# Performance work log

Hardware: AMD Instinct MI355X
Metric: run time of the kernel (lower is better)

## Reference

```python
import jax, jax.numpy as jnp
import numpy as np

N_HEADS = 16

def setup_inputs() -> dict:
    key = jax.random.key(0)
    k1, k2, k3 = jax.random.split(key, 3)
    B, T, C = 4, 2048, 1024
    x = jax.random.normal(k1, (B, T, C), dtype=jnp.float32)
    w_qkv = jax.random.normal(k2, (C, 3 * C), dtype=jnp.float32) * (1.0 / np.sqrt(C))
    w_out = jax.random.normal(k3, (C, C), dtype=jnp.float32) * (1.0 / np.sqrt(C))
    return {"x": x, "w_qkv": w_qkv, "w_out": w_out}

def reference(x, w_qkv, w_out):
    B, T, C = x.shape
    H = N_HEADS
    d_k = C // H
    qkv = x @ w_qkv                       # (B,T,3C)
    q, k, v = jnp.split(qkv, 3, axis=-1)
    # (B,H,T,d_k)
    q = q.reshape(B, T, H, d_k).transpose(0, 2, 1, 3)
    k = k.reshape(B, T, H, d_k).transpose(0, 2, 1, 3)
    v = v.reshape(B, T, H, d_k).transpose(0, 2, 1, 3)
    scale = 1.0 / np.sqrt(d_k)
    scores = jnp.einsum('bhqd,bhkd->bhqk', q, k) * scale  # (B,H,T,T)
    causal = jnp.triu(jnp.ones((T, T), dtype=bool), k=1)  # True = ignore
    scores = jnp.where(causal, -jnp.inf, scores)
    weights = jax.nn.softmax(scores, axis=-1)
    out = jnp.einsum('bhqk,bhkd->bhqd', weights, v)       # (B,H,T,d_k)
    out = out.transpose(0, 2, 1, 3).reshape(B, T, C)
    return out @ w_out
```

## Files before the change

kernel.cpp:

```cpp
#include <hip/hip_runtime.h>
#include <hip/hip_bf16.h>
#include <stdint.h>
#include <math.h>

typedef __bf16 bf16;
typedef __bf16 bf16x4 __attribute__((ext_vector_type(4)));
typedef __bf16 bf16x8 __attribute__((ext_vector_type(8)));
typedef float f32x4 __attribute__((ext_vector_type(4)));

#define BB 4
#define TT 2048
#define CC 1024
#define HH 16
#define DK 64

__device__ __forceinline__ void gl_lds16(const void* gsrc, void* ldst) {
    __builtin_amdgcn_global_load_lds(
        (__attribute__((address_space(1))) void*)(void*)(gsrc),
        (__attribute__((address_space(3))) void*)(ldst),
        16, 0, 0);
}

__global__ __launch_bounds__(256) void prep(
    const float* __restrict__ x, const float* __restrict__ wq,
    const float* __restrict__ wo, bf16* __restrict__ xbf,
    bf16* __restrict__ wqT, bf16* __restrict__ woT) {
    __shared__ bf16 tile[32][33];
    const int bid = blockIdx.x, tid = threadIdx.x;
    if (bid < 4096) {
        const int i = (bid * 256 + tid) * 8;
        const f32x4 a = *(const f32x4*)(x + i);
        const f32x4 b = *(const f32x4*)(x + i + 4);
        bf16x8 o;
#pragma unroll
        for (int j = 0; j < 4; ++j) { o[j] = (bf16)a[j]; o[j + 4] = (bf16)b[j]; }
        *(bf16x8*)(xbf + i) = o;
        return;
    }
    const float* in;
    bf16* out;
    int R, C, c0, r0;
    if (bid < 7168) {
        const int tb = bid - 4096;
        in = wq; out = wqT; R = 1024; C = 3072;
        c0 = (tb % 96) * 32; r0 = (tb / 96) * 32;
    } else {
        const int tb = bid - 7168;
        in = wo; out = woT; R = 1024; C = 1024;
        c0 = (tb % 32) * 32; r0 = (tb / 32) * 32;
    }
    const int tx = tid & 31, ty = tid >> 5;
#pragma unroll
    for (int i = 0; i < 32; i += 8)
        tile[ty + i][tx] = (bf16)in[(size_t)(r0 + ty + i) * C + c0 + tx];
    __syncthreads();
#pragma unroll
    for (int i = 0; i < 32; i += 8)
        out[(size_t)(c0 + ty + i) * R + r0 + tx] = tile[tx][ty + i];
}

template <int EPI>
__global__ __launch_bounds__(256) void gemm_bt(
    const bf16* __restrict__ A, const bf16* __restrict__ Bt,
    void* __restrict__ Cq, bf16* __restrict__ Kh, bf16* __restrict__ Vt,
    int M, int N, int K) {
    __shared__ bf16 As[128 * 32];
    __shared__ bf16 Bs[128 * 32];
    const int tid = threadIdx.x;
    const int w = tid >> 6, l = tid & 63;
    const int wm = w >> 1, wn = w & 1;
    const int m0 = blockIdx.y * 128, n0 = blockIdx.x * 128;
    const int lr4 = l >> 2, lc4 = (l & 3) * 8;
    const int lm = l & 15, lq = l >> 4;

    f32x4 acc[4][4] = {};

    for (int k0 = 0; k0 < K; k0 += 32) {
#pragma unroll
        for (int i = 0; i < 2; ++i) {
            const int j = w * 2 + i;
            gl_lds16(A + (size_t)(m0 + j * 16 + lr4) * K + k0 + lc4, As + j * 512);
            gl_lds16(Bt + (size_t)(n0 + j * 16 + lr4) * K + k0 + lc4, Bs + j * 512);
        }
        __syncthreads();
        bf16x8 af[4], bfr[4];
#pragma unroll
        for (int mi = 0; mi < 4; ++mi)
            af[mi] = *(const bf16x8*)(As + (wm * 64 + mi * 16 + lm) * 32 + lq * 8);
#pragma unroll
        for (int ni = 0; ni < 4; ++ni)
            bfr[ni] = *(const bf16x8*)(Bs + (wn * 64 + ni * 16 + lm) * 32 + lq * 8);
#pragma unroll
        for (int mi = 0; mi < 4; ++mi)
#pragma unroll
            for (int ni = 0; ni < 4; ++ni)
                acc[mi][ni] = __builtin_amdgcn_mfma_f32_16x16x32_bf16(
                    af[mi], bfr[ni], acc[mi][ni], 0, 0, 0);
        __syncthreads();
    }

    if (EPI == 0) {
#pragma unroll
        for (int mi = 0; mi < 4; ++mi) {
            const int row = m0 + wm * 64 + mi * 16 + lq * 4;
#pragma unroll
            for (int ni = 0; ni < 4; ++ni) {
                const int col = n0 + wn * 64 + ni * 16 + lm;
#pragma unroll
                for (int r = 0; r < 4; ++r)
                    ((float*)Cq)[(size_t)(row + r) * N + col] = acc[mi][ni][r];
            }
        }
    } else {
        bf16* Q = (bf16*)Cq;
#pragma unroll
        for (int ni = 0; ni < 4; ++ni) {
            const int c = n0 + wn * 64 + ni * 16 + lm;
            const int part = c >> 10;
            const int h = (c & 1023) >> 6;
            const int d = c & 63;
#pragma unroll
            for (int mi = 0; mi < 4; ++mi) {
                const int rowg = m0 + wm * 64 + mi * 16 + lq * 4;
#pragma unroll
                for (int r = 0; r < 4; ++r) {
                    const int rg = rowg + r;
                    const int b = rg >> 11, t = rg & 2047;
                    const bf16 v = (bf16)acc[mi][ni][r];
                    if (part == 0)
                        Q[((size_t)(b * HH + h) * TT + t) * DK + d] = v;
                    else if (part == 1)
                        Kh[((size_t)(b * HH + h) * TT + t) * DK + d] = v;
                    else
                        Vt[((size_t)(b * HH + h) * DK + d) * TT + t] = v;
                }
            }
        }
    }
}

#define PAD 72
__global__ __launch_bounds__(256, 3) void attn_kernel(
    const bf16* __restrict__ Qh, const bf16* __restrict__ Kh,
    const bf16* __restrict__ Vt, bf16* __restrict__ O) {
    __shared__ bf16 Ks[2][64 * PAD];
    __shared__ bf16 Vs[2][64 * PAD];
    __shared__ bf16 Ps[64 * PAD];
    const int tid = threadIdx.x, w = tid >> 6, l = tid & 63;
    const int lm = l & 15, lq = l >> 4;
    const int id = blockIdx.x;
    const int xcd = id & 7;
    const int rest = id >> 3;
    const int bh = xcd + 8 * (rest >> 4);
    const int p = rest & 15;
    const int b = bh >> 4, h = bh & 15;
    const bf16* Qb = Qh + (size_t)bh * TT * DK;
    const bf16* Kb = Kh + (size_t)bh * TT * DK;
    const bf16* Vb = Vt + (size_t)bh * DK * TT;
    const int srow = tid >> 3, scol = (tid & 7) * 8;

    const float smul = 0.125f * 1.44269504088896340736f;
    const int qts[2] = {p, 31 - p};

    bf16x8 kreg[2], vreg[2];
#pragma unroll
    for (int i = 0; i < 2; ++i) {
        kreg[i] = *(const bf16x8*)(Kb + (size_t)(srow + i * 32) * DK + scol);
        vreg[i] = *(const bf16x8*)(Vb + (size_t)(srow + i * 32) * TT + scol);
    }
    int buf = 0;

#pragma unroll
    for (int half = 0; half < 2; ++half) {
        const int qt = qts[half];
        const int q0 = qt * 64;
        const int qg = q0 + w * 16 + lm;

        bf16x8 qf[2];
#pragma unroll
        for (int ks = 0; ks < 2; ++ks)
            qf[ks] = *(const bf16x8*)(Qb + (size_t)(q0 + w * 16 + lm) * DK +
                                      ks * 32 + lq * 8);

        f32x4 oacc[4] = {};
        float lrun = 0.f;

        for (int kt = 0; kt <= qt; ++kt) {
#pragma unroll
            for (int i = 0; i < 2; ++i) {
                *(bf16x8*)(Ks[buf] + (srow + i * 32) * PAD + scol) = kreg[i];
                *(bf16x8*)(Vs[buf] + (srow + i * 32) * PAD + scol) = vreg[i];
            }
            __syncthreads();

            {
                int nkt = -1;
                if (kt < qt) nkt = kt + 1;
                else if (half == 0) nkt = 0;
                if (nkt >= 0) {
#pragma unroll
                    for (int i = 0; i < 2; ++i) {
                        kreg[i] = *(const bf16x8*)(
                            Kb + (size_t)(nkt * 64 + srow + i * 32) * DK + scol);
                        vreg[i] = *(const bf16x8*)(
                            Vb + (size_t)(srow + i * 32) * TT + nkt * 64 + scol);
                    }
                }
            }

            f32x4 st[4] = {};
#pragma unroll
            for (int ks = 0; ks < 2; ++ks) {
#pragma unroll
                for (int nb = 0; nb < 4; ++nb) {
                    const bf16x8 kf = *(const bf16x8*)(Ks[buf] + (nb * 16 + lm) * PAD +
                                                       ks * 32 + lq * 8);
                    st[nb] = __builtin_amdgcn_mfma_f32_16x16x32_bf16(
                        kf, qf[ks], st[nb], 0, 0, 0);
                }
            }

            const bool diag = (kt == qt);
#pragma unroll
            for (int nb = 0; nb < 4; ++nb) {
                bf16x4 pk;
#pragma unroll
                for (int r = 0; r < 4; ++r) {
                    float arg = fmaf(st[nb][r], smul, -20.f);
                    if (diag) {
                        const int keyg = kt * 64 + nb * 16 + lq * 4 + r;
                        if (keyg > qg) arg = -1e30f;
                    }
                    const float pv = exp2f(arg);
                    lrun += pv;
                    pk[r] = (bf16)pv;
                }
                *(bf16x4*)(Ps + (w * 16 + lm) * PAD + nb * 16 + lq * 4) = pk;
            }

#pragma unroll
            for (int ks = 0; ks < 2; ++ks) {
                const bf16x8 pf =
                    *(const bf16x8*)(Ps + (w * 16 + lm) * PAD + ks * 32 + lq * 8);
#pragma unroll
                for (int ni = 0; ni < 4; ++ni) {
                    const bf16x8 vf = *(const bf16x8*)(Vs[buf] + (ni * 16 + lm) * PAD +
                                                       ks * 32 + lq * 8);
                    oacc[ni] = __builtin_amdgcn_mfma_f32_16x16x32_bf16(
                        pf, vf, oacc[ni], 0, 0, 0);
                }
            }
            buf ^= 1;
        }

        lrun += __shfl_xor(lrun, 16);
        lrun += __shfl_xor(lrun, 32);
        float linv[4];
#pragma unroll
        for (int r = 0; r < 4; ++r) linv[r] = 1.0f / __shfl(lrun, lq * 4 + r);
#pragma unroll
        for (int ni = 0; ni < 4; ++ni) {
            const int col = h * 64 + ni * 16 + lm;
#pragma unroll
            for (int r = 0; r < 4; ++r) {
                const int t = q0 + w * 16 + lq * 4 + r;
                O[((size_t)(b * TT + t)) * CC + col] = (bf16)(oacc[ni][r] * linv[r]);
            }
        }
    }
}

extern "C" void kernel_launch(void* const* d_in, const int* in_sizes, int n_in,
                              void* d_out, int out_size, void* d_ws, size_t ws_size,
                              hipStream_t stream) {
    const float* x = (const float*)d_in[0];
    const float* w_qkv = (const float*)d_in[1];
    const float* w_out = (const float*)d_in[2];

    char* ws = (char*)d_ws;
    const size_t M1 = (size_t)1 << 20;
    bf16* Qh = (bf16*)(ws);
    bf16* Kh = (bf16*)(ws + 16 * M1);
    bf16* Vt = (bf16*)(ws + 32 * M1);
    bf16* Ob = (bf16*)(ws + 48 * M1);
    bf16* wqkvT = (bf16*)(ws + 64 * M1);
    bf16* woutT = (bf16*)(ws + 70 * M1);
    bf16* xbf = (bf16*)(ws + 72 * M1);

    prep<<<8192, 256, 0, stream>>>(x, w_qkv, w_out, xbf, wqkvT, woutT);
    gemm_bt<1><<<dim3(3072 / 128, 8192 / 128), 256, 0, stream>>>(
        xbf, wqkvT, Qh, Kh, Vt, 8192, 3072, 1024);
    attn_kernel<<<1024, 256, 0, stream>>>(Qh, Kh, Vt, Ob);
    gemm_bt<0><<<dim3(1024 / 128, 8192 / 128), 256, 0, stream>>>(
        Ob, woutT, (float*)d_out, nullptr, nullptr, 8192, 1024, 1024);
}
```

Before: 291.0 us.

## Replace GEMM with 256x256 double-buffered, swizzled-LDS pipelined kernel

The 128x128 single-buffer GEMM is replaced by a 512-thread 256x256-tile kernel with K-step 64. It double-buffers LDS, issues the next tile's global-to-LDS loads interleaved with MFMA quadrants using manual vmcnt waits and barriers, and XOR-swizzles the LDS layout to avoid bank conflicts. The aim is to hide memory latency and raise MFMA utilisation in both projections. In exchange it uses 128KB of LDS per block and more registers, which limits occupancy. For the output projection it launches only 128 blocks, which may underfill the GPU's compute units.

```diff
diff --git a/kernel.cpp b/kernel.cpp
--- a/kernel.cpp
+++ b/kernel.cpp
@@ -20,6 +20,13 @@
         (__attribute__((address_space(3))) void*)(ldst),
         16, 0, 0);
 }
+
+__device__ __forceinline__ void bar() {
+    asm volatile("" ::: "memory");
+    __builtin_amdgcn_s_barrier();
+    asm volatile("" ::: "memory");
+}
+#define VMCNT(N) asm volatile("s_waitcnt vmcnt(" #N ")" ::: "memory")
 
 __global__ __launch_bounds__(256) void prep(
     const float* __restrict__ x, const float* __restrict__ wq,
@@ -60,49 +67,109 @@
 }
 
 template <int EPI>
-__global__ __launch_bounds__(256) void gemm_bt(
+__global__ __launch_bounds__(512, 2) void gemm256(
     const bf16* __restrict__ A, const bf16* __restrict__ Bt,
     void* __restrict__ Cq, bf16* __restrict__ Kh, bf16* __restrict__ Vt,
     int M, int N, int K) {
-    __shared__ bf16 As[128 * 32];
-    __shared__ bf16 Bs[128 * 32];
+    __shared__ bf16 As[2][256 * 64];
+    __shared__ bf16 Bs[2][256 * 64];
     const int tid = threadIdx.x;
     const int w = tid >> 6, l = tid & 63;
-    const int wm = w >> 1, wn = w & 1;
-    const int m0 = blockIdx.y * 128, n0 = blockIdx.x * 128;
-    const int lr4 = l >> 2, lc4 = (l & 3) * 8;
+    const int wm = w >> 2, wn = w & 3;
     const int lm = l & 15, lq = l >> 4;
-
-    f32x4 acc[4][4] = {};
-
-    for (int k0 = 0; k0 < K; k0 += 32) {
-#pragma unroll
-        for (int i = 0; i < 2; ++i) {
-            const int j = w * 2 + i;
-            gl_lds16(A + (size_t)(m0 + j * 16 + lr4) * K + k0 + lc4, As + j * 512);
-            gl_lds16(Bt + (size_t)(n0 + j * 16 + lr4) * K + k0 + lc4, Bs + j * 512);
-        }
-        __syncthreads();
-        bf16x8 af[4], bfr[4];
-#pragma unroll
-        for (int mi = 0; mi < 4; ++mi)
-            af[mi] = *(const bf16x8*)(As + (wm * 64 + mi * 16 + lm) * 32 + lq * 8);
-#pragma unroll
-        for (int ni = 0; ni < 4; ++ni)
-            bfr[ni] = *(const bf16x8*)(Bs + (wn * 64 + ni * 16 + lm) * 32 + lq * 8);
-#pragma unroll
-        for (int mi = 0; mi < 4; ++mi)
-#pragma unroll
-            for (int ni = 0; ni < 4; ++ni)
-                acc[mi][ni] = __builtin_amdgcn_mfma_f32_16x16x32_bf16(
-                    af[mi], bfr[ni], acc[mi][ni], 0, 0, 0);
-        __syncthreads();
+    const int m0 = blockIdx.y * 256, n0 = blockIdx.x * 256;
+
+    const int srow_a = w * 8 + (l >> 3);
+    const int srow_b = (w & 3) * 8 + (w >> 2) * 64 + (l >> 3);
+    const int csw = ((l & 7) ^ (l >> 3)) * 8;
+    const bf16* agl = A + (size_t)(m0 + srow_a) * K + csw;
+    const bf16* bgl = Bt + (size_t)(n0 + srow_b) * K + csw;
+    const int wa = w * 8;
+    const int wb = (w & 3) * 8 + (w >> 2) * 64;
+
+    int aoff[2], boff[2];
+#pragma unroll
+    for (int ks = 0; ks < 2; ++ks) {
+        const int sl = (ks * 4 + lq) ^ (lm & 7);
+        aoff[ks] = (wm * 128 + lm) * 64 + sl * 8;
+        boff[ks] = (wn * 64 + lm) * 64 + sl * 8;
+    }
+
+    f32x4 acc[8][4] = {};
+    bf16x8 af[4][2], bfA[2][2], bfB[2][2];
+
+#define STGA(R, DSTA, KOFF) gl_lds16(agl + (size_t)(R) * K + (KOFF), (DSTA) + (wa + (R)) * 64)
+#define STGB(R, DSTB, KOFF) gl_lds16(bgl + (size_t)(R) * K + (KOFF), (DSTB) + (wb + (R)) * 64)
+#define LDA(MIH, SRC)                                                          \
+    _Pragma("unroll") for (int mi = 0; mi < 4; ++mi)                           \
+    _Pragma("unroll") for (int ks = 0; ks < 2; ++ks)                           \
+        af[mi][ks] = *(const bf16x8*)((SRC) + aoff[ks] + ((MIH) * 4 + mi) * 1024);
+#define LDB(BF, NIH, SRC)                                                      \
+    _Pragma("unroll") for (int ni = 0; ni < 2; ++ni)                           \
+    _Pragma("unroll") for (int ks = 0; ks < 2; ++ks)                           \
+        BF[ni][ks] = *(const bf16x8*)((SRC) + boff[ks] + ((NIH) * 2 + ni) * 1024);
+#define QMFMA(MIH, NIH, BF)                                                    \
+    __builtin_amdgcn_s_setprio(1);                                             \
+    _Pragma("unroll") for (int ks = 0; ks < 2; ++ks)                           \
+    _Pragma("unroll") for (int mi = 0; mi < 4; ++mi)                           \
+    _Pragma("unroll") for (int ni = 0; ni < 2; ++ni)                           \
+        acc[(MIH) * 4 + mi][(NIH) * 2 + ni] =                                  \
+            __builtin_amdgcn_mfma_f32_16x16x32_bf16(                           \
+                af[mi][ks], BF[ni][ks], acc[(MIH) * 4 + mi][(NIH) * 2 + ni],   \
+                0, 0, 0);                                                      \
+    __builtin_amdgcn_s_setprio(0);
+
+    bf16* A0 = &As[0][0]; bf16* A1 = &As[1][0];
+    bf16* B0 = &Bs[0][0]; bf16* B1 = &Bs[1][0];
+    const int NT = K >> 6;
+
+    STGA(0, A0, 0); STGA(128, A0, 0);
+    STGB(0, B0, 0); STGB(128, B0, 0);
+    STGB(32, B0, 0); STGB(160, B0, 0);
+    STGA(64, A0, 0); STGA(192, A0, 0);
+    VMCNT(4); bar();
+
+    for (int t = 0; t < NT - 1; ++t) {
+        const int bb = t & 1;
+        const bf16* Ac = bb ? A1 : A0; const bf16* Bc = bb ? B1 : B0;
+        bf16* An = bb ? A0 : A1;       bf16* Bn = bb ? B0 : B1;
+        const int k1 = (t + 1) << 6;
+        LDA(0, Ac); LDB(bfA, 0, Bc);
+        STGA(0, An, k1); STGA(128, An, k1);
+        bar();
+        QMFMA(0, 0, bfA);
+        VMCNT(4); bar();
+        LDB(bfB, 1, Bc);
+        STGB(0, Bn, k1); STGB(128, Bn, k1);
+        bar();
+        QMFMA(0, 1, bfB);
+        VMCNT(4); bar();
+        LDA(1, Ac);
+        STGB(32, Bn, k1); STGB(160, Bn, k1);
+        bar();
+        QMFMA(1, 1, bfB);
+        bar();
+        STGA(64, An, k1); STGA(192, An, k1);
+        bar();
+        QMFMA(1, 0, bfA);
+        VMCNT(4); bar();
+    }
+    {
+        const int bb = (NT - 1) & 1;
+        const bf16* Ac = bb ? A1 : A0; const bf16* Bc = bb ? B1 : B0;
+        LDA(0, Ac); LDB(bfA, 0, Bc);
+        bar(); QMFMA(0, 0, bfA); VMCNT(2); bar();
+        LDB(bfB, 1, Bc);
+        bar(); QMFMA(0, 1, bfB); VMCNT(0); bar();
+        LDA(1, Ac);
+        bar(); QMFMA(1, 1, bfB); bar();
+        QMFMA(1, 0, bfA);
     }
 
     if (EPI == 0) {
 #pragma unroll
-        for (int mi = 0; mi < 4; ++mi) {
-            const int row = m0 + wm * 64 + mi * 16 + lq * 4;
+        for (int mi = 0; mi < 8; ++mi) {
+            const int row = m0 + wm * 128 + mi * 16 + lq * 4;
 #pragma unroll
             for (int ni = 0; ni < 4; ++ni) {
                 const int col = n0 + wn * 64 + ni * 16 + lm;
@@ -120,8 +187,8 @@
             const int h = (c & 1023) >> 6;
             const int d = c & 63;
 #pragma unroll
-            for (int mi = 0; mi < 4; ++mi) {
-                const int rowg = m0 + wm * 64 + mi * 16 + lq * 4;
+            for (int mi = 0; mi < 8; ++mi) {
+                const int rowg = m0 + wm * 128 + mi * 16 + lq * 4;
 #pragma unroll
                 for (int r = 0; r < 4; ++r) {
                     const int rg = rowg + r;
@@ -137,6 +204,11 @@
             }
         }
     }
+#undef STGA
+#undef STGB
+#undef LDA
+#undef LDB
+#undef QMFMA
 }
 
 #define PAD 72
@@ -288,9 +360,9 @@
     bf16* xbf = (bf16*)(ws + 72 * M1);
 
     prep<<<8192, 256, 0, stream>>>(x, w_qkv, w_out, xbf, wqkvT, woutT);
-    gemm_bt<1><<<dim3(3072 / 128, 8192 / 128), 256, 0, stream>>>(
+    gemm256<1><<<dim3(3072 / 256, 8192 / 256), 512, 0, stream>>>(
         xbf, wqkvT, Qh, Kh, Vt, 8192, 3072, 1024);
     attn_kernel<<<1024, 256, 0, stream>>>(Qh, Kh, Vt, Ob);
-    gemm_bt<0><<<dim3(1024 / 128, 8192 / 128), 256, 0, stream>>>(
+    gemm256<0><<<dim3(1024 / 256, 8192 / 256), 512, 0, stream>>>(
         Ob, woutT, (float*)d_out, nullptr, nullptr, 8192, 1024, 1024);
 }
```

Result: faster. 279.2 us (-4.0%).
